# Kernel optimization log

Hardware: AMD Instinct MI355X
Metric: run time of the kernel (lower is better)

The kernel has to match this reference:

```python
import jax, jax.numpy as jnp
import numpy as np
from jax import lax

EXP_SCALING = 10.0

def setup_inputs() -> dict:
    key = jax.random.key(0)
    k1, _ = jax.random.split(key)
    B, H, T, D = 8, 16, 4096, 64
    k = jax.random.normal(k1, (B, H, T, D), dtype=jnp.float32)
    # nn.Parameter init: linspace(0.5, 5, H).view(1,H,1,1) / exp_scaling
    leaky_key_beta = (jnp.linspace(0.5, 5.0, H, dtype=jnp.float32) / EXP_SCALING).reshape(1, H, 1, 1)
    return {"k": k, "leaky_key_beta": leaky_key_beta}

def reference(k, leaky_key_beta):
    # alpha = exp(-|beta| * exp_scaling), shape [1,H,1,1] -> per-head scalar [H]
    alpha = jnp.exp(-jnp.abs(leaky_key_beta) * EXP_SCALING)[0, :, 0, 0]  # [H]
    a = alpha[None, :, None]  # [1,H,1] broadcast over (B,H,D)
    kT = jnp.moveaxis(k, 2, 0)  # [T,B,H,D]

    def step(carry, kt):  # carry,kt: [B,H,D]
        out = kt + a * carry  # out_t = k_t + alpha * out_{t-1}
        return out, out

    _, outs = lax.scan(step, jnp.zeros_like(kT[0]), kT)  # [T,B,H,D]
    return jnp.moveaxis(outs, 0, 2)  # [B,H,T,D]
```

## Files before the change

### kernel.cpp

```cpp
#include <hip/hip_runtime.h>
#include <math.h>


typedef float f32x4 __attribute__((ext_vector_type(4)));

#define T_LEN 4096
#define H_DIM 16
#define D4 16
#define CHUNK 16
#define WARM 16
#define CPB (T_LEN / CHUNK)

__device__ __forceinline__ f32x4 fma4(float a, f32x4 y, f32x4 kv) {
  f32x4 r;
  r.x = fmaf(a, y.x, kv.x);
  r.y = fmaf(a, y.y, kv.y);
  r.z = fmaf(a, y.z, kv.z);
  r.w = fmaf(a, y.w, kv.w);
  return r;
}

__global__ __launch_bounds__(256, 4) void leaky_avg_kernel(
    const f32x4* __restrict__ k,
    const float* __restrict__ beta,
    f32x4* __restrict__ out) {
  int idx = blockIdx.x * 256 + threadIdx.x;
  int d4 = idx & (D4 - 1);
  int g  = idx >> 4;
  int c  = g & (CPB - 1);
  int bh = g >> 8;
  int h  = bh & (H_DIM - 1);

  float a = expf(-fabsf(beta[h]) * 10.0f);

  const f32x4* kp = k   + (size_t)bh * (T_LEN * D4) + d4;
  f32x4*       op = out + (size_t)bh * (T_LEN * D4) + d4;
  int t0 = c * CHUNK;

  f32x4 y = {0.f, 0.f, 0.f, 0.f};
  f32x4 kb[WARM];

  if (t0 >= WARM) {
    const f32x4* hp = kp + (size_t)(t0 - WARM) * D4;
    #pragma unroll
    for (int s = 0; s < WARM; ++s) kb[s] = hp[s * D4];
    #pragma unroll
    for (int s = 0; s < WARM; ++s) y = fma4(a, y, kb[s]);
  }

  const f32x4* mp = kp + (size_t)t0 * D4;
  f32x4*       sp = op + (size_t)t0 * D4;
  #pragma unroll
  for (int s = 0; s < CHUNK; ++s) kb[s] = mp[s * D4];
  #pragma unroll
  for (int s = 0; s < CHUNK; ++s) {
    y = fma4(a, y, kb[s]);
    __builtin_nontemporal_store(y, &sp[s * D4]);
  }
}

extern "C" void kernel_launch(void* const* d_in, const int* in_sizes, int n_in,
                              void* d_out, int out_size, void* d_ws, size_t ws_size,
                              hipStream_t stream) {
  const f32x4* k    = (const f32x4*)d_in[0];
  const float* beta = (const float*)d_in[1];
  f32x4*       out  = (f32x4*)d_out;

  const int total = 128 * CPB * D4;
  leaky_avg_kernel<<<dim3(total / 256), dim3(256), 0, stream>>>(k, beta, out);
}
```

Baseline: 235.5 us.

## Stage key tiles into LDS via direct global-to-LDS loads and share halos

Each block now loads a contiguous tile of 128 rows plus a 16-row halo per (batch, head) into LDS using global_load_lds DMA. Threads run their truncated-warmup recurrence from LDS, so neighbouring chunks reuse the shared halo instead of each re-reading it from global memory, which cuts redundant global reads. Results are written back to LDS and then stored out as coalesced contiguous 16-byte writes. The cost is two extra barriers, an LDS round trip and fewer threads per block (128), which may reduce latency hiding. The nontemporal stores are also dropped.

```diff
diff --git a/kernel.cpp b/kernel.cpp
--- a/kernel.cpp
+++ b/kernel.cpp
@@ -6,10 +6,18 @@
 
 #define T_LEN 4096
 #define H_DIM 16
+#define ROW_B 256
 #define D4 16
-#define CHUNK 16
-#define WARM 16
-#define CPB (T_LEN / CHUNK)
+#define HALO 16
+#define MAIN_ROWS 128
+#define LDS_ROWS (MAIN_ROWS + HALO)
+#define LDS_BYTES (LDS_ROWS * ROW_B)
+#define THREADS 128
+#define NWAVES (THREADS / 64)
+#define WCHUNKS (LDS_BYTES / 1024)
+#define DMA_ITERS (WCHUNKS / NWAVES)
+#define BLOCKS_PER_BH (T_LEN / MAIN_ROWS)
+#define OUT_BYTES (MAIN_ROWS * ROW_B)
 
 __device__ __forceinline__ f32x4 fma4(float a, f32x4 y, f32x4 kv) {
   f32x4 r;
@@ -20,52 +28,90 @@
   return r;
 }
 
-__global__ __launch_bounds__(256, 4) void leaky_avg_kernel(
-    const f32x4* __restrict__ k,
+__global__ __launch_bounds__(THREADS, 2) void leaky_avg_kernel(
+    const float* __restrict__ k,
     const float* __restrict__ beta,
-    f32x4* __restrict__ out) {
-  int idx = blockIdx.x * 256 + threadIdx.x;
-  int d4 = idx & (D4 - 1);
-  int g  = idx >> 4;
-  int c  = g & (CPB - 1);
-  int bh = g >> 8;
-  int h  = bh & (H_DIM - 1);
+    float* __restrict__ out) {
+  __shared__ __align__(16) unsigned char lds_raw[LDS_BYTES];
 
-  float a = expf(-fabsf(beta[h]) * 10.0f);
+  const int tid = threadIdx.x;
+  const int bid = blockIdx.x;
+  const int bh  = bid >> 5;
+  const int bc  = bid & (BLOCKS_PER_BH - 1);
+  const int h   = bh & (H_DIM - 1);
+  const float a = expf(-fabsf(beta[h]) * 10.0f);
 
-  const f32x4* kp = k   + (size_t)bh * (T_LEN * D4) + d4;
-  f32x4*       op = out + (size_t)bh * (T_LEN * D4) + d4;
-  int t0 = c * CHUNK;
+  const size_t bh_byte = (size_t)bh * ((size_t)T_LEN * ROW_B);
+  const int t0_blk = bc * MAIN_ROWS;
+
+  {
+    const int wave = tid >> 6;
+    const int lane = tid & 63;
+    const char* kc = (const char*)k + bh_byte;
+    #pragma unroll
+    for (int i = 0; i < DMA_ITERS; ++i) {
+      const int q    = i * NWAVES + wave;
+      const int loff = q * 1024 + lane * 16;
+      int goff = (t0_blk - HALO) * ROW_B + loff;
+      if (goff < 0) goff += HALO * ROW_B;
+      __builtin_amdgcn_global_load_lds(
+          (const __attribute__((address_space(1))) void*)(kc + goff),
+          (__attribute__((address_space(3))) void*)(lds_raw + loff),
+          16, 0, 0);
+    }
+  }
+  asm volatile("s_waitcnt vmcnt(0)" ::: "memory");
+  __syncthreads();
+
+  const int d4i   = tid & (D4 - 1);
+  const int cl    = tid >> 4;
+  const int rbase = cl * 16;
+  const f32x4* ldsv = (const f32x4*)lds_raw;
 
   f32x4 y = {0.f, 0.f, 0.f, 0.f};
-  f32x4 kb[WARM];
-
-  if (t0 >= WARM) {
-    const f32x4* hp = kp + (size_t)(t0 - WARM) * D4;
+  if (!(bc == 0 && cl == 0)) {
+    f32x4 hreg[HALO];
     #pragma unroll
-    for (int s = 0; s < WARM; ++s) kb[s] = hp[s * D4];
+    for (int s = 0; s < HALO; ++s) hreg[s] = ldsv[(rbase + s) * D4 + d4i];
     #pragma unroll
-    for (int s = 0; s < WARM; ++s) y = fma4(a, y, kb[s]);
+    for (int s = 0; s < HALO; ++s) y = fma4(a, y, hreg[s]);
   }
 
-  const f32x4* mp = kp + (size_t)t0 * D4;
-  f32x4*       sp = op + (size_t)t0 * D4;
-  #pragma unroll
-  for (int s = 0; s < CHUNK; ++s) kb[s] = mp[s * D4];
-  #pragma unroll
-  for (int s = 0; s < CHUNK; ++s) {
-    y = fma4(a, y, kb[s]);
-    __builtin_nontemporal_store(y, &sp[s * D4]);
+  f32x4 yreg[16];
+  {
+    f32x4 mreg[16];
+    #pragma unroll
+    for (int s = 0; s < 16; ++s) mreg[s] = ldsv[(rbase + HALO + s) * D4 + d4i];
+    #pragma unroll
+    for (int s = 0; s < 16; ++s) { y = fma4(a, y, mreg[s]); yreg[s] = y; }
+  }
+
+  __syncthreads();
+
+  {
+    f32x4* ldsw = (f32x4*)lds_raw;
+    #pragma unroll
+    for (int s = 0; s < 16; ++s) ldsw[(rbase + HALO + s) * D4 + d4i] = yreg[s];
+  }
+  __syncthreads();
+
+  {
+    const char* lsrc = (const char*)lds_raw + HALO * ROW_B;
+    char* odst = (char*)out + bh_byte + (size_t)t0_blk * ROW_B;
+    #pragma unroll
+    for (int i = 0; i < OUT_BYTES / (THREADS * 16); ++i) {
+      const int o = i * (THREADS * 16) + tid * 16;
+      *(f32x4*)(odst + o) = *(const f32x4*)(lsrc + o);
+    }
   }
 }
 
 extern "C" void kernel_launch(void* const* d_in, const int* in_sizes, int n_in,
                               void* d_out, int out_size, void* d_ws, size_t ws_size,
                               hipStream_t stream) {
-  const f32x4* k    = (const f32x4*)d_in[0];
+  const float* k    = (const float*)d_in[0];
   const float* beta = (const float*)d_in[1];
-  f32x4*       out  = (f32x4*)d_out;
+  float*       out  = (float*)d_out;
 
-  const int total = 128 * CPB * D4;
-  leaky_avg_kernel<<<dim3(total / 256), dim3(256), 0, stream>>>(k, beta, out);
+  leaky_avg_kernel<<<dim3(128 * BLOCKS_PER_BH), dim3(THREADS), 0, stream>>>(k, beta, out);
 }
```

New measurement: 232.8 us. Within noise of the previous version (-1.1%).
